# Performance work log

Measured on AMD Instinct MI355X. Metric: run time of the kernel, lower is better.

## Reference

```python
import jax, jax.numpy as jnp
import numpy as np

N_HEADS = 16
MASK_VAL = -50000.0  # module sets masked scores to this value (not -inf)


def setup_inputs() -> dict:
    key = jax.random.key(0)
    kq, kk, kv = jax.random.split(key, 3)
    b, n, d_model = 2, 2048, 2048
    q = jax.random.normal(kq, (b, n, d_model), dtype=jnp.float32)
    k = jax.random.normal(kk, (b, n, d_model), dtype=jnp.float32)
    v = jax.random.normal(kv, (b, n, d_model), dtype=jnp.float32)
    return {"q": q, "k": k, "v": v}


def reference(q, k, v):
    b, n, d_model = q.shape
    h = N_HEADS
    dh = d_model // h
    scale = dh ** -0.5
    # 'b n (h d) -> b h n d'
    qh = q.reshape(b, n, h, dh).transpose(0, 2, 1, 3)
    kh = k.reshape(b, n, h, dh).transpose(0, 2, 1, 3)
    vh = v.reshape(b, n, h, dh).transpose(0, 2, 1, 3)
    # dots = (q * scale) @ k^T  -> [b, h, n, n]
    dots = jnp.einsum('bhid,bhjd->bhij', qh * scale, kh)
    # per-chunk triu_indices(csz, l, offset=i*csz+1) == global causal mask j > i,
    # with masked entries SET to MASK_VAL
    i_idx = jnp.arange(n)[:, None]
    j_idx = jnp.arange(n)[None, :]
    dots = jnp.where(j_idx > i_idx, MASK_VAL, dots)
    attn = jax.nn.softmax(dots, axis=-1)
    out = jnp.einsum('bhij,bhjd->bhid', attn, vh)
    # 'b h n d -> b n (h d)'
    return out.transpose(0, 2, 1, 3).reshape(b, n, d_model)
```

## Files before the change

kernel.cpp:

```cpp
#include <hip/hip_runtime.h>
#include <hip/hip_bf16.h>

#define B_SZ   2
#define N_SEQ  2048
#define NH     16
#define DH     128
#define DM     2048
#define QB     128
#define KVB    64
#define NQT    (N_SEQ / QB)
#define MASK_VAL (-50000.0f)

typedef short bf16x8 __attribute__((ext_vector_type(8)));
typedef short bf16x4 __attribute__((ext_vector_type(4)));
typedef float f32x4  __attribute__((ext_vector_type(4)));
typedef float f32x16 __attribute__((ext_vector_type(16)));
typedef unsigned u32;
typedef unsigned u32x4 __attribute__((ext_vector_type(4)));

__device__ __forceinline__ short f2bf(float x) {
  unsigned u = __builtin_bit_cast(unsigned, x);
  return (short)((u + 0x7fffu + ((u >> 16) & 1u)) >> 16);
}
__device__ __forceinline__ u32 pk2(float a, float b) {
  return (u32)(unsigned short)f2bf(a) | ((u32)(unsigned short)f2bf(b) << 16);
}

__global__ __launch_bounds__(256, 2)
void attn_fwd(const float* __restrict__ q, const float* __restrict__ k,
              const float* __restrict__ v, float* __restrict__ out) {
  __shared__ __align__(16) char  ldsK[64 * 256];
  __shared__ __align__(16) char  ldsVT[128 * 128];
  __shared__ __align__(16) float ldsA[4 * 32];

  const int tid  = threadIdx.x;
  const int lane = tid & 63;
  const int w    = tid >> 6;
  const int h    = lane >> 5;
  const int il   = lane & 31;

  const int bid = blockIdx.x;
  const int bh  = bid & 31;
  const int qt  = (bid < 256) ? (bid >> 5) : (NQT - 1 - ((bid - 256) >> 5));
  const int b   = bh >> 4;
  const int hd  = bh & 15;
  const int q0  = qt * QB;
  const int wq0 = q0 + w * 32;
  const int irow = wq0 + il;

  const float scale = 0.08838834764831845f;

  const float* kb = k + (size_t)b * N_SEQ * DM + hd * DH;
  const float* vb = v + (size_t)b * N_SEQ * DM + hd * DH;

  bf16x8 qf[8];
  {
    const float* qr = q + ((size_t)b * N_SEQ + irow) * DM + hd * DH + h * 8;
    #pragma unroll
    for (int s = 0; s < 8; ++s) {
      float4 a = *(const float4*)(qr + s * 16);
      float4 c = *(const float4*)(qr + s * 16 + 4);
      qf[s][0] = f2bf(a.x * scale); qf[s][1] = f2bf(a.y * scale);
      qf[s][2] = f2bf(a.z * scale); qf[s][3] = f2bf(a.w * scale);
      qf[s][4] = f2bf(c.x * scale); qf[s][5] = f2bf(c.y * scale);
      qf[s][6] = f2bf(c.z * scale); qf[s][7] = f2bf(c.w * scale);
    }
  }

  float m_ = -INFINITY, ll = 0.f;
  f32x16 o[4];
  #pragma unroll
  for (int dt = 0; dt < 4; ++dt)
    #pragma unroll
    for (int r = 0; r < 16; ++r) o[dt][r] = 0.f;

  const int kswz = (il & 7) << 4;
  const int d_   = tid & 127;
  const int jh   = tid >> 7;

  const int nt = 2 * qt + 2;
  for (int t = 0; t < nt; ++t) {
    const int jt = t * KVB;
    if (t) __syncthreads();

    {
      const float* kt = kb + (size_t)jt * DM;
      #pragma unroll
      for (int i = 0; i < 8; ++i) {
        int idx = i * 256 + tid;
        int row = idx >> 5;
        int c4  = idx & 31;
        float4 f = *(const float4*)(kt + (size_t)row * DM + c4 * 4);
        bf16x4 hv;
        hv[0] = f2bf(f.x); hv[1] = f2bf(f.y); hv[2] = f2bf(f.z); hv[3] = f2bf(f.w);
        *(bf16x4*)(ldsK + row * 256 + ((c4 * 8) ^ ((row & 7) << 4))) = hv;
      }
    }
    {
      const float* vt = vb + (size_t)jt * DM;
      #pragma unroll
      for (int t2 = 0; t2 < 4; ++t2) {
        int j0 = jh * 32 + t2 * 8;
        bf16x8 hv;
        #pragma unroll
        for (int jj = 0; jj < 8; ++jj)
          hv[jj] = f2bf(vt[(size_t)(j0 + jj) * DM + d_]);
        *(bf16x8*)(ldsVT + d_ * 128 + ((j0 * 2) ^ ((d_ & 7) << 4))) = hv;
      }
    }
    __syncthreads();

    if (jt > wq0 + 31) continue;
    const bool act1 = (jt + 32 <= wq0 + 31);

    f32x16 sc0 = {0,0,0,0,0,0,0,0,0,0,0,0,0,0,0,0};
    f32x16 sc1 = {0,0,0,0,0,0,0,0,0,0,0,0,0,0,0,0};
    #pragma unroll
    for (int s = 0; s < 8; ++s) {
      bf16x8 kf0 = *(const bf16x8*)(ldsK + il * 256 + ((s * 32 + h * 16) ^ kswz));
      sc0 = __builtin_amdgcn_mfma_f32_32x32x16_bf16(kf0, qf[s], sc0, 0, 0, 0);
    }
    if (act1) {
      #pragma unroll
      for (int s = 0; s < 8; ++s) {
        bf16x8 kf1 = *(const bf16x8*)(ldsK + (32 + il) * 256 + ((s * 32 + h * 16) ^ kswz));
        sc1 = __builtin_amdgcn_mfma_f32_32x32x16_bf16(kf1, qf[s], sc1, 0, 0, 0);
      }
    }

    if (jt + 31 > wq0) {
      #pragma unroll
      for (int r = 0; r < 16; ++r) {
        int j = jt + (r & 3) + 8 * (r >> 2) + 4 * h;
        sc0[r] = (j > irow) ? MASK_VAL : sc0[r];
      }
    }
    if (act1 && (jt + 63 > wq0)) {
      #pragma unroll
      for (int r = 0; r < 16; ++r) {
        int j = jt + 32 + (r & 3) + 8 * (r >> 2) + 4 * h;
        sc1[r] = (j > irow) ? MASK_VAL : sc1[r];
      }
    }

    float pmax = sc0[0];
    #pragma unroll
    for (int r = 1; r < 16; ++r) pmax = fmaxf(pmax, sc0[r]);
    if (act1) {
      #pragma unroll
      for (int r = 0; r < 16; ++r) pmax = fmaxf(pmax, sc1[r]);
    }
    pmax = fmaxf(pmax, __shfl_xor(pmax, 32));
    const float mnew = fmaxf(m_, pmax);

    #pragma unroll
    for (int r = 0; r < 16; ++r) sc0[r] = __expf(sc0[r] - mnew);
    if (act1) {
      #pragma unroll
      for (int r = 0; r < 16; ++r) sc1[r] = __expf(sc1[r] - mnew);
    }
    float rs = 0.f;
    #pragma unroll
    for (int r = 0; r < 16; ++r) rs += sc0[r];
    if (act1) {
      #pragma unroll
      for (int r = 0; r < 16; ++r) rs += sc1[r];
    }
    rs += __shfl_xor(rs, 32);

    const float alpha = __expf(m_ - mnew);
    ll = ll * alpha + rs;
    const bool changed = mnew > m_;
    m_ = mnew;

    if (__any(changed)) {
      ldsA[w * 32 + il] = alpha;
      f32x4 av[4];
      #pragma unroll
      for (int m = 0; m < 4; ++m)
        av[m] = *(const f32x4*)(ldsA + w * 32 + 8 * m + 4 * h);
      #pragma unroll
      for (int dt = 0; dt < 4; ++dt)
        #pragma unroll
        for (int m = 0; m < 4; ++m)
          #pragma unroll
          for (int r2 = 0; r2 < 4; ++r2)
            o[dt][m * 4 + r2] *= av[m][r2];
    }

    bf16x8 pa0[2], pa1[2];
    {
      #pragma unroll
      for (int ss = 0; ss < 2; ++ss) {
        u32 w0 = pk2(sc0[8 * ss + 0], sc0[8 * ss + 1]);
        u32 w1 = pk2(sc0[8 * ss + 2], sc0[8 * ss + 3]);
        u32 w2 = pk2(sc0[8 * ss + 4], sc0[8 * ss + 5]);
        u32 w3 = pk2(sc0[8 * ss + 6], sc0[8 * ss + 7]);
        asm volatile("v_permlane32_swap_b32 %0, %1" : "+v"(w0), "+v"(w2));
        asm volatile("v_permlane32_swap_b32 %0, %1" : "+v"(w1), "+v"(w3));
        u32x4 t4 = {w0, w1, w2, w3};
        pa0[ss] = __builtin_bit_cast(bf16x8, t4);
      }
    }
    if (act1) {
      #pragma unroll
      for (int ss = 0; ss < 2; ++ss) {
        u32 w0 = pk2(sc1[8 * ss + 0], sc1[8 * ss + 1]);
        u32 w1 = pk2(sc1[8 * ss + 2], sc1[8 * ss + 3]);
        u32 w2 = pk2(sc1[8 * ss + 4], sc1[8 * ss + 5]);
        u32 w3 = pk2(sc1[8 * ss + 6], sc1[8 * ss + 7]);
        asm volatile("v_permlane32_swap_b32 %0, %1" : "+v"(w0), "+v"(w2));
        asm volatile("v_permlane32_swap_b32 %0, %1" : "+v"(w1), "+v"(w3));
        u32x4 t4 = {w0, w1, w2, w3};
        pa1[ss] = __builtin_bit_cast(bf16x8, t4);
      }
    }

    #pragma unroll
    for (int dt = 0; dt < 4; ++dt) {
      const int drow = dt * 32 + il;
      char* vrow = ldsVT + drow * 128;
      {
        bf16x8 vf0 = *(const bf16x8*)(vrow + ((0 * 32 + 16 * h) ^ kswz));
        o[dt] = __builtin_amdgcn_mfma_f32_32x32x16_bf16(pa0[0], vf0, o[dt], 0, 0, 0);
        bf16x8 vf1 = *(const bf16x8*)(vrow + ((1 * 32 + 16 * h) ^ kswz));
        o[dt] = __builtin_amdgcn_mfma_f32_32x32x16_bf16(pa0[1], vf1, o[dt], 0, 0, 0);
      }
      if (act1) {
        bf16x8 vf2 = *(const bf16x8*)(vrow + ((2 * 32 + 16 * h) ^ kswz));
        o[dt] = __builtin_amdgcn_mfma_f32_32x32x16_bf16(pa1[0], vf2, o[dt], 0, 0, 0);
        bf16x8 vf3 = *(const bf16x8*)(vrow + ((3 * 32 + 16 * h) ^ kswz));
        o[dt] = __builtin_amdgcn_mfma_f32_32x32x16_bf16(pa1[1], vf3, o[dt], 0, 0, 0);
      }
    }
  }

  ldsA[w * 32 + il] = 1.0f / ll;
  f32x4 iv[4];
  #pragma unroll
  for (int m = 0; m < 4; ++m)
    iv[m] = *(const f32x4*)(ldsA + w * 32 + 8 * m + 4 * h);

  float* ob = out + ((size_t)b * N_SEQ + wq0) * DM + hd * DH;
  #pragma unroll
  for (int dt = 0; dt < 4; ++dt) {
    #pragma unroll
    for (int m = 0; m < 4; ++m) {
      #pragma unroll
      for (int r2 = 0; r2 < 4; ++r2) {
        int i_loc = 8 * m + 4 * h + r2;
        ob[(size_t)i_loc * DM + dt * 32 + il] = o[dt][m * 4 + r2] * iv[m][r2];
      }
    }
  }
}

extern "C" void kernel_launch(void* const* d_in, const int* in_sizes, int n_in,
                              void* d_out, int out_size, void* d_ws, size_t ws_size,
                              hipStream_t stream) {
  const float* q = (const float*)d_in[0];
  const float* k = (const float*)d_in[1];
  const float* v = (const float*)d_in[2];
  float* out = (float*)d_out;
  dim3 grid(B_SZ * NH * NQT);
  attn_fwd<<<grid, 256, 0, stream>>>(q, k, v, out);
}
```

Measured before the change: 110.5 us.

## Double-buffer K/V tiles with register prefetch, lazy rescale, and hardware bf16 pack

Global loads for the next K/V tile are issued into registers before computing on the current tile, then converted and written into a second LDS buffer after compute. This hides global-load latency behind the MFMA and softmax work and removes one barrier per iteration. It also adds a lazy max update that only rescales the accumulator when the row max grows by more than a threshold, swaps software bf16 rounding for v_cvt_pk_bf16_f32, and raises wave priority around the MFMA blocks. In exchange it doubles LDS use and adds 64 prefetch registers, which may hurt occupancy at 2 blocks per CU.

```diff
diff --git a/kernel.cpp b/kernel.cpp
--- a/kernel.cpp
+++ b/kernel.cpp
@@ -12,25 +12,23 @@
 #define MASK_VAL (-50000.0f)
 
 typedef short bf16x8 __attribute__((ext_vector_type(8)));
-typedef short bf16x4 __attribute__((ext_vector_type(4)));
 typedef float f32x4  __attribute__((ext_vector_type(4)));
 typedef float f32x16 __attribute__((ext_vector_type(16)));
 typedef unsigned u32;
+typedef unsigned u32x2 __attribute__((ext_vector_type(2)));
 typedef unsigned u32x4 __attribute__((ext_vector_type(4)));
 
-__device__ __forceinline__ short f2bf(float x) {
-  unsigned u = __builtin_bit_cast(unsigned, x);
-  return (short)((u + 0x7fffu + ((u >> 16) & 1u)) >> 16);
-}
 __device__ __forceinline__ u32 pk2(float a, float b) {
-  return (u32)(unsigned short)f2bf(a) | ((u32)(unsigned short)f2bf(b) << 16);
+  u32 r;
+  asm("v_cvt_pk_bf16_f32 %0, %1, %2" : "=v"(r) : "v"(a), "v"(b));
+  return r;
 }
 
 __global__ __launch_bounds__(256, 2)
 void attn_fwd(const float* __restrict__ q, const float* __restrict__ k,
               const float* __restrict__ v, float* __restrict__ out) {
-  __shared__ __align__(16) char  ldsK[64 * 256];
-  __shared__ __align__(16) char  ldsVT[128 * 128];
+  __shared__ __align__(16) char  ldsK[2 * 64 * 256];
+  __shared__ __align__(16) char  ldsVT[2 * 128 * 128];
   __shared__ __align__(16) float ldsA[4 * 32];
 
   const int tid  = threadIdx.x;
@@ -53,6 +51,55 @@
   const float* kb = k + (size_t)b * N_SEQ * DM + hd * DH;
   const float* vb = v + (size_t)b * N_SEQ * DM + hd * DH;
 
+  float4 kr[8];
+  float  vr[32];
+  const int d_ = tid & 127;
+  const int jh = tid >> 7;
+
+  auto issue_loads = [&](int jt) {
+    const float* kt = kb + (size_t)jt * DM;
+    #pragma unroll
+    for (int i = 0; i < 8; ++i) {
+      int idx = i * 256 + tid;
+      int row = idx >> 5;
+      int c4  = idx & 31;
+      kr[i] = *(const float4*)(kt + (size_t)row * DM + c4 * 4);
+    }
+    const float* vt = vb + (size_t)jt * DM;
+    #pragma unroll
+    for (int t2 = 0; t2 < 4; ++t2) {
+      int j0 = jh * 32 + t2 * 8;
+      #pragma unroll
+      for (int jj = 0; jj < 8; ++jj)
+        vr[t2 * 8 + jj] = vt[(size_t)(j0 + jj) * DM + d_];
+    }
+  };
+
+  auto write_lds = [&](int buf) {
+    char* K  = ldsK  + buf * 16384;
+    char* VT = ldsVT + buf * 16384;
+    #pragma unroll
+    for (int i = 0; i < 8; ++i) {
+      int idx = i * 256 + tid;
+      int row = idx >> 5;
+      int c4  = idx & 31;
+      u32x2 p;
+      p[0] = pk2(kr[i].x, kr[i].y);
+      p[1] = pk2(kr[i].z, kr[i].w);
+      *(u32x2*)(K + row * 256 + ((c4 * 8) ^ ((row & 7) << 4))) = p;
+    }
+    #pragma unroll
+    for (int t2 = 0; t2 < 4; ++t2) {
+      int j0 = jh * 32 + t2 * 8;
+      u32x4 p;
+      p[0] = pk2(vr[t2 * 8 + 0], vr[t2 * 8 + 1]);
+      p[1] = pk2(vr[t2 * 8 + 2], vr[t2 * 8 + 3]);
+      p[2] = pk2(vr[t2 * 8 + 4], vr[t2 * 8 + 5]);
+      p[3] = pk2(vr[t2 * 8 + 6], vr[t2 * 8 + 7]);
+      *(u32x4*)(VT + d_ * 128 + ((j0 * 2) ^ ((d_ & 7) << 4))) = p;
+    }
+  };
+
   bf16x8 qf[8];
   {
     const float* qr = q + ((size_t)b * N_SEQ + irow) * DM + hd * DH + h * 8;
@@ -60,10 +107,12 @@
     for (int s = 0; s < 8; ++s) {
       float4 a = *(const float4*)(qr + s * 16);
       float4 c = *(const float4*)(qr + s * 16 + 4);
-      qf[s][0] = f2bf(a.x * scale); qf[s][1] = f2bf(a.y * scale);
-      qf[s][2] = f2bf(a.z * scale); qf[s][3] = f2bf(a.w * scale);
-      qf[s][4] = f2bf(c.x * scale); qf[s][5] = f2bf(c.y * scale);
-      qf[s][6] = f2bf(c.z * scale); qf[s][7] = f2bf(c.w * scale);
+      u32x4 t4;
+      t4[0] = pk2(a.x * scale, a.y * scale);
+      t4[1] = pk2(a.z * scale, a.w * scale);
+      t4[2] = pk2(c.x * scale, c.y * scale);
+      t4[3] = pk2(c.z * scale, c.w * scale);
+      qf[s] = __builtin_bit_cast(bf16x8, t4);
     }
   }
 
@@ -75,121 +124,101 @@
     for (int r = 0; r < 16; ++r) o[dt][r] = 0.f;
 
   const int kswz = (il & 7) << 4;
-  const int d_   = tid & 127;
-  const int jh   = tid >> 7;
 
   const int nt = 2 * qt + 2;
+
+  issue_loads(0);
+  write_lds(0);
+  __syncthreads();
+
+  int cur = 0;
   for (int t = 0; t < nt; ++t) {
     const int jt = t * KVB;
-    if (t) __syncthreads();
-
-    {
-      const float* kt = kb + (size_t)jt * DM;
-      #pragma unroll
-      for (int i = 0; i < 8; ++i) {
-        int idx = i * 256 + tid;
-        int row = idx >> 5;
-        int c4  = idx & 31;
-        float4 f = *(const float4*)(kt + (size_t)row * DM + c4 * 4);
-        bf16x4 hv;
-        hv[0] = f2bf(f.x); hv[1] = f2bf(f.y); hv[2] = f2bf(f.z); hv[3] = f2bf(f.w);
-        *(bf16x4*)(ldsK + row * 256 + ((c4 * 8) ^ ((row & 7) << 4))) = hv;
-      }
-    }
-    {
-      const float* vt = vb + (size_t)jt * DM;
-      #pragma unroll
-      for (int t2 = 0; t2 < 4; ++t2) {
-        int j0 = jh * 32 + t2 * 8;
-        bf16x8 hv;
-        #pragma unroll
-        for (int jj = 0; jj < 8; ++jj)
-          hv[jj] = f2bf(vt[(size_t)(j0 + jj) * DM + d_]);
-        *(bf16x8*)(ldsVT + d_ * 128 + ((j0 * 2) ^ ((d_ & 7) << 4))) = hv;
-      }
-    }
-    __syncthreads();
-
-    if (jt > wq0 + 31) continue;
-    const bool act1 = (jt + 32 <= wq0 + 31);
-
-    f32x16 sc0 = {0,0,0,0,0,0,0,0,0,0,0,0,0,0,0,0};
-    f32x16 sc1 = {0,0,0,0,0,0,0,0,0,0,0,0,0,0,0,0};
-    #pragma unroll
-    for (int s = 0; s < 8; ++s) {
-      bf16x8 kf0 = *(const bf16x8*)(ldsK + il * 256 + ((s * 32 + h * 16) ^ kswz));
-      sc0 = __builtin_amdgcn_mfma_f32_32x32x16_bf16(kf0, qf[s], sc0, 0, 0, 0);
-    }
-    if (act1) {
+    const bool have_next = (t + 1 < nt);
+    if (have_next) issue_loads(jt + KVB);
+
+    if (jt <= wq0 + 31) {
+      char* K  = ldsK  + cur * 16384;
+      char* VT = ldsVT + cur * 16384;
+      const bool act1 = (jt + 32 <= wq0 + 31);
+
+      f32x16 sc0 = {0,0,0,0,0,0,0,0,0,0,0,0,0,0,0,0};
+      f32x16 sc1 = {0,0,0,0,0,0,0,0,0,0,0,0,0,0,0,0};
+      __builtin_amdgcn_s_setprio(1);
       #pragma unroll
       for (int s = 0; s < 8; ++s) {
-        bf16x8 kf1 = *(const bf16x8*)(ldsK + (32 + il) * 256 + ((s * 32 + h * 16) ^ kswz));
-        sc1 = __builtin_amdgcn_mfma_f32_32x32x16_bf16(kf1, qf[s], sc1, 0, 0, 0);
-      }
-    }
-
-    if (jt + 31 > wq0) {
-      #pragma unroll
-      for (int r = 0; r < 16; ++r) {
-        int j = jt + (r & 3) + 8 * (r >> 2) + 4 * h;
-        sc0[r] = (j > irow) ? MASK_VAL : sc0[r];
-      }
-    }
-    if (act1 && (jt + 63 > wq0)) {
-      #pragma unroll
-      for (int r = 0; r < 16; ++r) {
-        int j = jt + 32 + (r & 3) + 8 * (r >> 2) + 4 * h;
-        sc1[r] = (j > irow) ? MASK_VAL : sc1[r];
-      }
-    }
-
-    float pmax = sc0[0];
-    #pragma unroll
-    for (int r = 1; r < 16; ++r) pmax = fmaxf(pmax, sc0[r]);
-    if (act1) {
-      #pragma unroll
-      for (int r = 0; r < 16; ++r) pmax = fmaxf(pmax, sc1[r]);
-    }
-    pmax = fmaxf(pmax, __shfl_xor(pmax, 32));
-    const float mnew = fmaxf(m_, pmax);
-
-    #pragma unroll
-    for (int r = 0; r < 16; ++r) sc0[r] = __expf(sc0[r] - mnew);
-    if (act1) {
-      #pragma unroll
-      for (int r = 0; r < 16; ++r) sc1[r] = __expf(sc1[r] - mnew);
-    }
-    float rs = 0.f;
-    #pragma unroll
-    for (int r = 0; r < 16; ++r) rs += sc0[r];
-    if (act1) {
-      #pragma unroll
-      for (int r = 0; r < 16; ++r) rs += sc1[r];
-    }
-    rs += __shfl_xor(rs, 32);
-
-    const float alpha = __expf(m_ - mnew);
-    ll = ll * alpha + rs;
-    const bool changed = mnew > m_;
-    m_ = mnew;
-
-    if (__any(changed)) {
-      ldsA[w * 32 + il] = alpha;
-      f32x4 av[4];
-      #pragma unroll
-      for (int m = 0; m < 4; ++m)
-        av[m] = *(const f32x4*)(ldsA + w * 32 + 8 * m + 4 * h);
-      #pragma unroll
-      for (int dt = 0; dt < 4; ++dt)
+        bf16x8 kf0 = *(const bf16x8*)(K + il * 256 + ((s * 32 + h * 16) ^ kswz));
+        sc0 = __builtin_amdgcn_mfma_f32_32x32x16_bf16(kf0, qf[s], sc0, 0, 0, 0);
+      }
+      if (act1) {
+        #pragma unroll
+        for (int s = 0; s < 8; ++s) {
+          bf16x8 kf1 = *(const bf16x8*)(K + (32 + il) * 256 + ((s * 32 + h * 16) ^ kswz));
+          sc1 = __builtin_amdgcn_mfma_f32_32x32x16_bf16(kf1, qf[s], sc1, 0, 0, 0);
+        }
+      }
+      __builtin_amdgcn_s_setprio(0);
+
+      if (jt + 31 > wq0) {
+        #pragma unroll
+        for (int r = 0; r < 16; ++r) {
+          int j = jt + (r & 3) + 8 * (r >> 2) + 4 * h;
+          sc0[r] = (j > irow) ? MASK_VAL : sc0[r];
+        }
+      }
+      if (act1 && (jt + 63 > wq0)) {
+        #pragma unroll
+        for (int r = 0; r < 16; ++r) {
+          int j = jt + 32 + (r & 3) + 8 * (r >> 2) + 4 * h;
+          sc1[r] = (j > irow) ? MASK_VAL : sc1[r];
+        }
+      }
+
+      float pmax = sc0[0];
+      #pragma unroll
+      for (int r = 1; r < 16; ++r) pmax = fmaxf(pmax, sc0[r]);
+      if (act1) {
+        #pragma unroll
+        for (int r = 0; r < 16; ++r) pmax = fmaxf(pmax, sc1[r]);
+      }
+      pmax = fmaxf(pmax, __shfl_xor(pmax, 32));
+
+      if (!__all(pmax <= m_ + 8.f)) {
+        const float mnew = fmaxf(m_, pmax);
+        const float alpha = __expf(m_ - mnew);
+        ll *= alpha;
+        m_ = mnew;
+        ldsA[w * 32 + il] = alpha;
+        f32x4 av[4];
         #pragma unroll
         for (int m = 0; m < 4; ++m)
+          av[m] = *(const f32x4*)(ldsA + w * 32 + 8 * m + 4 * h);
+        #pragma unroll
+        for (int dt = 0; dt < 4; ++dt)
           #pragma unroll
-          for (int r2 = 0; r2 < 4; ++r2)
-            o[dt][m * 4 + r2] *= av[m][r2];
-    }
-
-    bf16x8 pa0[2], pa1[2];
-    {
+          for (int m = 0; m < 4; ++m)
+            #pragma unroll
+            for (int r2 = 0; r2 < 4; ++r2)
+              o[dt][m * 4 + r2] *= av[m][r2];
+      }
+
+      #pragma unroll
+      for (int r = 0; r < 16; ++r) sc0[r] = __expf(sc0[r] - m_);
+      if (act1) {
+        #pragma unroll
+        for (int r = 0; r < 16; ++r) sc1[r] = __expf(sc1[r] - m_);
+      }
+      float rs = 0.f;
+      #pragma unroll
+      for (int r = 0; r < 16; ++r) rs += sc0[r];
+      if (act1) {
+        #pragma unroll
+        for (int r = 0; r < 16; ++r) rs += sc1[r];
+      }
+      rs += __shfl_xor(rs, 32);
+      ll += rs;
+
+      bf16x8 pa0[2], pa1[2];
       #pragma unroll
       for (int ss = 0; ss < 2; ++ss) {
         u32 w0 = pk2(sc0[8 * ss + 0], sc0[8 * ss + 1]);
@@ -201,37 +230,43 @@
         u32x4 t4 = {w0, w1, w2, w3};
         pa0[ss] = __builtin_bit_cast(bf16x8, t4);
       }
-    }
-    if (act1) {
-      #pragma unroll
-      for (int ss = 0; ss < 2; ++ss) {
-        u32 w0 = pk2(sc1[8 * ss + 0], sc1[8 * ss + 1]);
-        u32 w1 = pk2(sc1[8 * ss + 2], sc1[8 * ss + 3]);
-        u32 w2 = pk2(sc1[8 * ss + 4], sc1[8 * ss + 5]);
-        u32 w3 = pk2(sc1[8 * ss + 6], sc1[8 * ss + 7]);
-        asm volatile("v_permlane32_swap_b32 %0, %1" : "+v"(w0), "+v"(w2));
-        asm volatile("v_permlane32_swap_b32 %0, %1" : "+v"(w1), "+v"(w3));
-        u32x4 t4 = {w0, w1, w2, w3};
-        pa1[ss] = __builtin_bit_cast(bf16x8, t4);
-      }
-    }
-
-    #pragma unroll
-    for (int dt = 0; dt < 4; ++dt) {
-      const int drow = dt * 32 + il;
-      char* vrow = ldsVT + drow * 128;
-      {
+      if (act1) {
+        #pragma unroll
+        for (int ss = 0; ss < 2; ++ss) {
+          u32 w0 = pk2(sc1[8 * ss + 0], sc1[8 * ss + 1]);
+          u32 w1 = pk2(sc1[8 * ss + 2], sc1[8 * ss + 3]);
+          u32 w2 = pk2(sc1[8 * ss + 4], sc1[8 * ss + 5]);
+          u32 w3 = pk2(sc1[8 * ss + 6], sc1[8 * ss + 7]);
+          asm volatile("v_permlane32_swap_b32 %0, %1" : "+v"(w0), "+v"(w2));
+          asm volatile("v_permlane32_swap_b32 %0, %1" : "+v"(w1), "+v"(w3));
+          u32x4 t4 = {w0, w1, w2, w3};
+          pa1[ss] = __builtin_bit_cast(bf16x8, t4);
+        }
+      }
+
+      __builtin_amdgcn_s_setprio(1);
+      #pragma unroll
+      for (int dt = 0; dt < 4; ++dt) {
+        const int drow = dt * 32 + il;
+        char* vrow = VT + drow * 128;
         bf16x8 vf0 = *(const bf16x8*)(vrow + ((0 * 32 + 16 * h) ^ kswz));
         o[dt] = __builtin_amdgcn_mfma_f32_32x32x16_bf16(pa0[0], vf0, o[dt], 0, 0, 0);
         bf16x8 vf1 = *(const bf16x8*)(vrow + ((1 * 32 + 16 * h) ^ kswz));
         o[dt] = __builtin_amdgcn_mfma_f32_32x32x16_bf16(pa0[1], vf1, o[dt], 0, 0, 0);
-      }
-      if (act1) {
-        bf16x8 vf2 = *(const bf16x8*)(vrow + ((2 * 32 + 16 * h) ^ kswz));
-        o[dt] = __builtin_amdgcn_mfma_f32_32x32x16_bf16(pa1[0], vf2, o[dt], 0, 0, 0);
-        bf16x8 vf3 = *(const bf16x8*)(vrow + ((3 * 32 + 16 * h) ^ kswz));
-        o[dt] = __builtin_amdgcn_mfma_f32_32x32x16_bf16(pa1[1], vf3, o[dt], 0, 0, 0);
-      }
+        if (act1) {
+          bf16x8 vf2 = *(const bf16x8*)(vrow + ((2 * 32 + 16 * h) ^ kswz));
+          o[dt] = __builtin_amdgcn_mfma_f32_32x32x16_bf16(pa1[0], vf2, o[dt], 0, 0, 0);
+          bf16x8 vf3 = *(const bf16x8*)(vrow + ((3 * 32 + 16 * h) ^ kswz));
+          o[dt] = __builtin_amdgcn_mfma_f32_32x32x16_bf16(pa1[1], vf3, o[dt], 0, 0, 0);
+        }
+      }
+      __builtin_amdgcn_s_setprio(0);
+    }
+
+    if (have_next) {
+      write_lds(cur ^ 1);
+      __syncthreads();
+      cur ^= 1;
     }
   }
 
```

Result: slower. 387.1 us (+250.2%).
